# Optimization experiments

Measured on AMD Instinct MI355X. Metric: run time of the kernel, lower is better.

## Reference

```python
import jax, jax.numpy as jnp
import numpy as np
import math

B, N, M = 4, 2048, 2048
DIM_Q = DIM_K = DIM_V = 1024
H = 16

def setup_inputs() -> dict:
    key = jax.random.key(0)
    ks = jax.random.split(key, 10)
    s = 0.02
    return {
        "Q": jax.random.normal(ks[0], (B, N, DIM_Q), jnp.float32),
        "K": jax.random.normal(ks[1], (B, M, DIM_K), jnp.float32),
        "Wq": jax.random.normal(ks[2], (DIM_V, DIM_Q), jnp.float32) * s,
        "bq": jax.random.normal(ks[3], (DIM_V,), jnp.float32) * s,
        "Wk": jax.random.normal(ks[4], (DIM_V, DIM_K), jnp.float32) * s,
        "bk": jax.random.normal(ks[5], (DIM_V,), jnp.float32) * s,
        "Wv": jax.random.normal(ks[6], (DIM_V, DIM_K), jnp.float32) * s,
        "bv": jax.random.normal(ks[7], (DIM_V,), jnp.float32) * s,
        "Wo": jax.random.normal(ks[8], (DIM_V, DIM_V), jnp.float32) * s,
        "bo": jax.random.normal(ks[9], (DIM_V,), jnp.float32) * s,
    }

def reference(Q, K, Wq, bq, Wk, bk, Wv, bv, Wo, bo):
    d = DIM_V // H  # head dim
    Qp = Q @ Wq.T + bq            # [B,N,DIM_V]
    Kp = K @ Wk.T + bk            # [B,M,DIM_V]
    Vp = K @ Wv.T + bv            # [B,M,DIM_V]
    # split heads: [B,T,H,d] -> [B,H,T,d]
    Qh = Qp.reshape(B, N, H, d).transpose(0, 2, 1, 3)
    Kh = Kp.reshape(B, M, H, d).transpose(0, 2, 1, 3)
    Vh = Vp.reshape(B, M, H, d).transpose(0, 2, 1, 3)
    # NOTE: original scales by sqrt(dim_V), not sqrt(head_dim)
    scores = jnp.einsum('bhnd,bhmd->bhnm', Qh, Kh) / math.sqrt(DIM_V)
    A = jax.nn.softmax(scores, axis=-1)
    Oh = Qh + jnp.einsum('bhnm,bhmd->bhnd', A, Vh)   # residual with projected Q
    O = Oh.transpose(0, 2, 1, 3).reshape(B, N, DIM_V)
    O = O + jax.nn.relu(O @ Wo.T + bo)
    return O
```

## Files before the change

kernel.cpp:

```cpp
#include <hip/hip_runtime.h>
#include <cstddef>
#include <cstdint>


typedef unsigned short ushort_t;
typedef __attribute__((ext_vector_type(8))) short bf16x8;
typedef __attribute__((ext_vector_type(4))) float floatx4;
typedef __attribute__((ext_vector_type(2))) float f32x2;
typedef __attribute__((ext_vector_type(2))) __bf16 b16x2;
typedef __attribute__((ext_vector_type(4))) unsigned short us4;

__device__ __forceinline__ ushort_t f2bf(float x) {
  union { float f; unsigned u; } v; v.f = x;
  unsigned r = v.u + 0x7FFFu + ((v.u >> 16) & 1u);
  return (ushort_t)(r >> 16);
}
__device__ __forceinline__ float bf2f(ushort_t x) {
  union { unsigned u; float f; } v; v.u = ((unsigned)x) << 16;
  return v.f;
}
__device__ __forceinline__ unsigned pk2(float a, float b) {
  union { float f; unsigned u; } x, y; x.f = a; y.f = b;
  return __builtin_amdgcn_perm(y.u + 0x8000u, x.u + 0x8000u, 0x07060302u);
}
__device__ __forceinline__ unsigned pk2c(float a, float b) {
  union { b16x2 v; unsigned u; } r;
  r.v = __builtin_convertvector((f32x2){a, b}, b16x2);
  return r.u;
}
__device__ __forceinline__ floatx4 mfma16(bf16x8 a, bf16x8 b, floatx4 c) {
  return __builtin_amdgcn_mfma_f32_16x16x32_bf16(a, b, c, 0, 0, 0);
}
__device__ __forceinline__ void gld_lds16(const void* g, void* l) {
  __builtin_amdgcn_global_load_lds(
      (const __attribute__((address_space(1))) unsigned int*)g,
      (__attribute__((address_space(3))) unsigned int*)l, 16, 0, 0);
}

__global__ void cvt6(const float* __restrict__ i0, const float* __restrict__ i1,
                     const float* __restrict__ i2, const float* __restrict__ i3,
                     const float* __restrict__ i4, const float* __restrict__ i5,
                     ushort_t* __restrict__ o0, ushort_t* __restrict__ o1,
                     ushort_t* __restrict__ o2, ushort_t* __restrict__ o3,
                     ushort_t* __restrict__ o4, ushort_t* __restrict__ o5) {
  int z = blockIdx.z;
  const float* in = z == 0 ? i0 : z == 1 ? i1 : z == 2 ? i2 : z == 3 ? i3 : z == 4 ? i4 : i5;
  ushort_t* out = z == 0 ? o0 : z == 1 ? o1 : z == 2 ? o2 : z == 3 ? o3 : z == 4 ? o4 : o5;
  int n8 = (z < 2) ? 1048576 : 131072;
  int i = blockIdx.x * 256 + threadIdx.x;
  if (i < n8) {
    const float4* p = (const float4*)in + (size_t)i * 2;
    float4 a = p[0], b = p[1];
    uint4 o;
    o.x = pk2(a.x, a.y); o.y = pk2(a.z, a.w);
    o.z = pk2(b.x, b.y); o.w = pk2(b.z, b.w);
    *((uint4*)out + i) = o;
  }
}

__global__ __launch_bounds__(256, 2)
void gemm_qkv(const ushort_t* __restrict__ Qb, const ushort_t* __restrict__ Kb,
              const ushort_t* __restrict__ Wqb, const ushort_t* __restrict__ Wkb,
              const ushort_t* __restrict__ Wvb,
              const float* __restrict__ bq, const float* __restrict__ bk,
              const float* __restrict__ bv,
              ushort_t* __restrict__ Qp, ushort_t* __restrict__ Kp,
              ushort_t* __restrict__ Vt)
{
  const int Kd = 1024, Nn = 1024;
  const int z = blockIdx.z;
  const ushort_t* Ab = (z == 0) ? Qb : Kb;
  const ushort_t* Bw = (z == 0) ? Wqb : (z == 1) ? Wkb : Wvb;
  const float* bias  = (z == 0) ? bq : (z == 1) ? bk : bv;

  __shared__ __align__(16) ushort_t As[2][8192];
  __shared__ __align__(16) ushort_t Bs[2][8192];
  const int tid = threadIdx.x;
  const int lane = tid & 63, wave = tid >> 6;
  const int wm = (wave >> 1) * 64, wn = (wave & 1) * 64;
  const int rq = lane & 15, kg = lane >> 4;

  const int wg = blockIdx.x, xcd = wg & 7, slot = wg >> 3;
  const int by = xcd * 8 + (slot >> 3);
  const int bx = slot & 7;
  const int row0 = by * 128, col0 = bx * 128;

  const int st_sub = lane >> 3;
  const int st_cs  = (lane & 7) ^ st_sub;

  auto stageAB = [&](int k0, int bufi) {
#pragma unroll
    for (int r = 0; r < 4; ++r) {
      int i = wave * 4 + r;
      int row = i * 8 + st_sub;
      gld_lds16(Ab + (size_t)(row0 + row) * Kd + k0 + st_cs * 8, &As[bufi][i * 512]);
      gld_lds16(Bw + (size_t)(col0 + row) * Kd + k0 + st_cs * 8, &Bs[bufi][i * 512]);
    }
  };

  floatx4 acc[4][4];
#pragma unroll
  for (int i = 0; i < 4; ++i)
#pragma unroll
    for (int j = 0; j < 4; ++j) acc[i][j] = (floatx4){0.f, 0.f, 0.f, 0.f};

  stageAB(0, 0);
  __syncthreads();

  int cur = 0;
  for (int kt = 0; kt < 16; ++kt) {
    if (kt < 15) stageAB((kt + 1) * 64, cur ^ 1);
#pragma unroll
    for (int kq = 0; kq < 2; ++kq) {
      bf16x8 af[4], bfr[4];
#pragma unroll
      for (int mi = 0; mi < 4; ++mi)
        af[mi] = *(const bf16x8*)&As[cur][(wm + mi*16 + rq) * 64 + (((kq*4 + kg) ^ (rq & 7)) * 8)];
#pragma unroll
      for (int ni = 0; ni < 4; ++ni)
        bfr[ni] = *(const bf16x8*)&Bs[cur][(wn + ni*16 + rq) * 64 + (((kq*4 + kg) ^ (rq & 7)) * 8)];
#pragma unroll
      for (int mi = 0; mi < 4; ++mi)
#pragma unroll
        for (int ni = 0; ni < 4; ++ni)
          acc[mi][ni] = mfma16(af[mi], bfr[ni], acc[mi][ni]);
    }
    __syncthreads();
    cur ^= 1;
  }

  float bv4[4];
#pragma unroll
  for (int ni = 0; ni < 4; ++ni) bv4[ni] = bias[col0 + wn + ni*16 + rq];

  if (z < 2) {
    ushort_t* Cb = (z == 0) ? Qp : Kp;
#pragma unroll
    for (int mi = 0; mi < 4; ++mi)
#pragma unroll
      for (int ni = 0; ni < 4; ++ni)
#pragma unroll
        for (int rr = 0; rr < 4; ++rr) {
          int row = row0 + wm + mi*16 + kg*4 + rr;
          int col = col0 + wn + ni*16 + rq;
          Cb[(size_t)row * Nn + col] = f2bf(acc[mi][ni][rr] + bv4[ni]);
        }
  } else {
#pragma unroll
    for (int mi = 0; mi < 4; ++mi)
#pragma unroll
      for (int ni = 0; ni < 4; ++ni) {
        int col = col0 + wn + ni*16 + rq;
        int h = col >> 6, dvb = (col >> 4) & 3;
        int kvg = row0 + wm + (mi >> 1) * 32;
        int bI = kvg >> 11, kv = kvg & 2047;
        int t = kv >> 7, c = (kv >> 5) & 3;
        size_t addr = (size_t)(bI * 16 + h) * 131072 + t * 8192
                    + (c * 4 + dvb) * 512 + (kg * 16 + rq) * 8 + (mi & 1) * 4;
        us4 o = { f2bf(acc[mi][ni][0] + bv4[ni]), f2bf(acc[mi][ni][1] + bv4[ni]),
                  f2bf(acc[mi][ni][2] + bv4[ni]), f2bf(acc[mi][ni][3] + bv4[ni]) };
        *(us4*)(Vt + addr) = o;
      }
  }
}

__global__ __launch_bounds__(256, 2)
void gemm_out(const ushort_t* __restrict__ Ob, const ushort_t* __restrict__ Bw,
              const float* __restrict__ bias, float* __restrict__ Out)
{
  const int Kd = 1024, Nn = 1024;
  __shared__ __align__(16) ushort_t As[2][8192];
  __shared__ __align__(16) ushort_t Bs[2][8192];
  const int tid = threadIdx.x;
  const int lane = tid & 63, wave = tid >> 6;
  const int wm = (wave >> 1) * 64, wn = (wave & 1) * 64;
  const int rq = lane & 15, kg = lane >> 4;

  const int wg = blockIdx.x, xcd = wg & 7, slot = wg >> 3;
  const int by = xcd * 8 + (slot >> 3);
  const int bx = slot & 7;
  const int row0 = by * 128, col0 = bx * 128;

  const int st_sub = lane >> 3;
  const int st_cs  = (lane & 7) ^ st_sub;

  auto stageAB = [&](int k0, int bufi) {
#pragma unroll
    for (int r = 0; r < 4; ++r) {
      int i = wave * 4 + r;
      int row = i * 8 + st_sub;
      gld_lds16(Ob + (size_t)(row0 + row) * Kd + k0 + st_cs * 8, &As[bufi][i * 512]);
      gld_lds16(Bw + (size_t)(col0 + row) * Kd + k0 + st_cs * 8, &Bs[bufi][i * 512]);
    }
  };

  floatx4 acc[4][4];
#pragma unroll
  for (int i = 0; i < 4; ++i)
#pragma unroll
    for (int j = 0; j < 4; ++j) acc[i][j] = (floatx4){0.f, 0.f, 0.f, 0.f};

  stageAB(0, 0);
  __syncthreads();

  int cur = 0;
  for (int kt = 0; kt < 16; ++kt) {
    if (kt < 15) stageAB((kt + 1) * 64, cur ^ 1);
#pragma unroll
    for (int kq = 0; kq < 2; ++kq) {
      bf16x8 af[4], bfr[4];
#pragma unroll
      for (int mi = 0; mi < 4; ++mi)
        af[mi] = *(const bf16x8*)&As[cur][(wm + mi*16 + rq) * 64 + (((kq*4 + kg) ^ (rq & 7)) * 8)];
#pragma unroll
      for (int ni = 0; ni < 4; ++ni)
        bfr[ni] = *(const bf16x8*)&Bs[cur][(wn + ni*16 + rq) * 64 + (((kq*4 + kg) ^ (rq & 7)) * 8)];
#pragma unroll
      for (int mi = 0; mi < 4; ++mi)
#pragma unroll
        for (int ni = 0; ni < 4; ++ni)
          acc[mi][ni] = mfma16(af[mi], bfr[ni], acc[mi][ni]);
    }
    __syncthreads();
    cur ^= 1;
  }

  float bv4[4];
#pragma unroll
  for (int ni = 0; ni < 4; ++ni) bv4[ni] = bias[col0 + wn + ni*16 + rq];
#pragma unroll
  for (int mi = 0; mi < 4; ++mi)
#pragma unroll
    for (int ni = 0; ni < 4; ++ni)
#pragma unroll
      for (int rr = 0; rr < 4; ++rr) {
        int row = row0 + wm + mi*16 + kg*4 + rr;
        int col = col0 + wn + ni*16 + rq;
        size_t idx = (size_t)row * Nn + col;
        float pre = acc[mi][ni][rr] + bv4[ni];
        Out[idx] = bf2f(Ob[idx]) + (pre > 0.f ? pre : 0.f);
      }
}

__global__ __launch_bounds__(256, 2)
void attn_kernel(const ushort_t* __restrict__ Qp,
                 const ushort_t* __restrict__ Kp,
                 const ushort_t* __restrict__ Vt,
                 ushort_t* __restrict__ Ob)
{
  const float sc2 = 0.045084439f;
  const int wg = blockIdx.x, xcd = wg & 7, slot = wg >> 3;
  const int bh = xcd * 8 + (slot >> 4);
  const int qt = slot & 15;
  const int b = bh >> 4, h = bh & 15;
  const int q0 = qt * 128;

  __shared__ __align__(16) ushort_t Ks[2][8192];

  const int tid = threadIdx.x, lane = tid & 63, wq = tid >> 6;
  const int rq = lane & 15, kg = lane >> 4;

  const size_t qkbase = (size_t)(b * 2048) * 1024 + h * 64;
  const ushort_t* vbase = Vt + (size_t)bh * 131072 + lane * 8;

  const int sg_sub = lane >> 3;
  const int sg_csk = (lane & 7) ^ sg_sub;

#pragma unroll
  for (int r = 0; r < 4; ++r) {
    int i = wq * 4 + r;
    int row = i * 8 + sg_sub;
    gld_lds16(Qp + qkbase + (size_t)(q0 + row) * 1024 + sg_csk * 8, &Ks[1][i * 512]);
  }
  __syncthreads();

  auto stage = [&](int kt, int bufi) {
    const int kv0 = kt * 128;
#pragma unroll
    for (int r = 0; r < 4; ++r) {
      int i = wq * 4 + r;
      int rowk = i * 8 + sg_sub;
      gld_lds16(Kp + qkbase + (size_t)(kv0 + rowk) * 1024 + sg_csk * 8,
                &Ks[bufi][i * 512]);
    }
  };
  stage(0, 0);

  bf16x8 aq[2][2];
#pragma unroll
  for (int ni = 0; ni < 2; ++ni)
#pragma unroll
    for (int kq = 0; kq < 2; ++kq) {
      int row = wq * 32 + ni * 16 + rq;
      int ch = (kq * 4 + kg) ^ (rq & 7);
      bf16x8 t = *(const bf16x8*)&Ks[1][row * 64 + ch * 8];
#pragma unroll
      for (int e = 0; e < 8; ++e)
        t[e] = (short)f2bf(bf2f((ushort_t)t[e]) * sc2);
      aq[ni][kq] = t;
    }

  bf16x8 ones;
#pragma unroll
  for (int e = 0; e < 8; ++e) ones[e] = (short)0x3F80;

  const floatx4 zf = (floatx4){0.f, 0.f, 0.f, 0.f};

  floatx4 oacc[2][4];
  floatx4 lacc[2];
#pragma unroll
  for (int nb = 0; nb < 2; ++nb) {
    lacc[nb] = (floatx4){0.f,0.f,0.f,0.f};
#pragma unroll
    for (int dvb = 0; dvb < 4; ++dvb) oacc[nb][dvb] = (floatx4){0.f,0.f,0.f,0.f};
  }

  __syncthreads();

  int cur = 0;
#pragma unroll 2
  for (int kt = 0; kt < 16; ++kt) {
    const ushort_t* vtile = vbase + kt * 8192;

    bf16x8 vfa[16];
#pragma unroll
    for (int j = 0; j < 16; ++j)
      vfa[j] = *(const bf16x8*)(vtile + j * 512);

    if (kt < 15) stage(kt + 1, cur ^ 1);

    floatx4 s[8][2];
    __builtin_amdgcn_s_setprio(1);
    {
      bf16x8 ak[8];
#pragma unroll
      for (int mi = 0; mi < 8; ++mi)
        ak[mi] = *(const bf16x8*)&Ks[cur][(mi * 16 + rq) * 64 + ((kg ^ (rq & 7)) * 8)];
#pragma unroll
      for (int mi = 0; mi < 8; ++mi)
#pragma unroll
        for (int ni = 0; ni < 2; ++ni)
          s[mi][ni] = mfma16(ak[mi], aq[ni][0], zf);
#pragma unroll
      for (int mi = 0; mi < 8; ++mi)
        ak[mi] = *(const bf16x8*)&Ks[cur][(mi * 16 + rq) * 64 + (((4 + kg) ^ (rq & 7)) * 8)];
#pragma unroll
      for (int mi = 0; mi < 8; ++mi)
#pragma unroll
        for (int ni = 0; ni < 2; ++ni)
          s[mi][ni] = mfma16(ak[mi], aq[ni][1], s[mi][ni]);
    }
    __builtin_amdgcn_s_setprio(0);

#pragma unroll
    for (int mi = 0; mi < 2; ++mi)
#pragma unroll
      for (int ni = 0; ni < 2; ++ni)
#pragma unroll
        for (int rr = 0; rr < 4; ++rr)
          s[mi][ni][rr] = __builtin_amdgcn_exp2f(s[mi][ni][rr]);

#pragma unroll
    for (int c = 0; c < 4; ++c) {
      union { unsigned u[4]; bf16x8 v; } pa0, pa1;
      pa0.u[0] = pk2c(s[2*c  ][0][0], s[2*c  ][0][1]);
      pa0.u[1] = pk2c(s[2*c  ][0][2], s[2*c  ][0][3]);
      pa0.u[2] = pk2c(s[2*c+1][0][0], s[2*c+1][0][1]);
      pa0.u[3] = pk2c(s[2*c+1][0][2], s[2*c+1][0][3]);
      pa1.u[0] = pk2c(s[2*c  ][1][0], s[2*c  ][1][1]);
      pa1.u[1] = pk2c(s[2*c  ][1][2], s[2*c  ][1][3]);
      pa1.u[2] = pk2c(s[2*c+1][1][0], s[2*c+1][1][1]);
      pa1.u[3] = pk2c(s[2*c+1][1][2], s[2*c+1][1][3]);
      __builtin_amdgcn_s_setprio(1);
#pragma unroll
      for (int dvb = 0; dvb < 4; ++dvb) {
        oacc[0][dvb] = mfma16(pa0.v, vfa[c*4+dvb], oacc[0][dvb]);
        oacc[1][dvb] = mfma16(pa1.v, vfa[c*4+dvb], oacc[1][dvb]);
      }
      lacc[0] = mfma16(pa0.v, ones, lacc[0]);
      lacc[1] = mfma16(pa1.v, ones, lacc[1]);
      __builtin_amdgcn_s_setprio(0);
      if (c < 3) {
#pragma unroll
        for (int mi = 2*c + 2; mi < 2*c + 4; ++mi)
#pragma unroll
          for (int ni = 0; ni < 2; ++ni)
#pragma unroll
            for (int rr = 0; rr < 4; ++rr)
              s[mi][ni][rr] = __builtin_amdgcn_exp2f(s[mi][ni][rr]);
      }
    }

    __syncthreads();
    cur ^= 1;
  }

#pragma unroll
  for (int nb = 0; nb < 2; ++nb)
#pragma unroll
    for (int rr = 0; rr < 4; ++rr) {
      int row = wq * 32 + nb * 16 + kg * 4 + rr;
      float linv = 1.0f / lacc[nb][rr];
#pragma unroll
      for (int dvb = 0; dvb < 4; ++dvb) {
        int col = dvb * 16 + rq;
        size_t idx = qkbase + (size_t)(q0 + row) * 1024 + col;
        Ob[idx] = f2bf(oacc[nb][dvb][rr] * linv + bf2f(Qp[idx]));
      }
    }
}

extern "C" void kernel_launch(void* const* d_in, const int* in_sizes, int n_in,
                              void* d_out, int out_size, void* d_ws, size_t ws_size,
                              hipStream_t stream)
{
  const float* Q  = (const float*)d_in[0];
  const float* K  = (const float*)d_in[1];
  const float* Wq = (const float*)d_in[2];
  const float* bq = (const float*)d_in[3];
  const float* Wk = (const float*)d_in[4];
  const float* bk = (const float*)d_in[5];
  const float* Wv = (const float*)d_in[6];
  const float* bv = (const float*)d_in[7];
  const float* Wo = (const float*)d_in[8];
  const float* bo = (const float*)d_in[9];
  float* Out = (float*)d_out;

  ushort_t* ws = (ushort_t*)d_ws;
  const size_t E = (size_t)8192 * 1024;
  const size_t WSZ = (size_t)1024 * 1024;
  ushort_t* Qb  = ws;
  ushort_t* Kb  = ws + E;
  ushort_t* Qp  = ws + 2*E;
  ushort_t* Kp  = ws + 3*E;
  ushort_t* Vt  = ws + 4*E;
  ushort_t* Wqb = ws + 5*E;
  ushort_t* Wkb = ws + 5*E + WSZ;
  ushort_t* Wvb = ws + 5*E + 2*WSZ;
  ushort_t* Wob = ws + 5*E + 3*WSZ;
  ushort_t* Ob  = Qb;

  cvt6<<<dim3(4096, 1, 6), 256, 0, stream>>>(Q, K, Wq, Wk, Wv, Wo,
                                             Qb, Kb, Wqb, Wkb, Wvb, Wob);

  dim3 blk(256);
  gemm_qkv<<<dim3(512, 1, 3), blk, 0, stream>>>(Qb, Kb, Wqb, Wkb, Wvb,
                                                bq, bk, bv, Qp, Kp, Vt);
  attn_kernel<<<dim3(1024), blk, 0, stream>>>(Qp, Kp, Vt, Ob);
  gemm_out<<<dim3(512), blk, 0, stream>>>(Ob, Wob, bo, Out);
}
```

Before: 277.5 us.

## Split attention key tile into two halves to cut registers and raise occupancy

Each 128-key tile in the attention inner loop is now processed as two 64-key halves. Scores, exp and the PV MFMAs run per half, and the V fragments are loaded in two batches of 8 instead of 16 at once. The manual unroll of 2 is dropped and launch bounds rise from 2 to 3 waves-per-SIMD occupancy, so the compiler must fit more waves per CU. This risks spills or exposed V global-load latency, because the second V batch is fetched mid-iteration with less time to hide it.

```diff
diff --git a/kernel.cpp b/kernel.cpp
--- a/kernel.cpp
+++ b/kernel.cpp
@@ -242,7 +242,7 @@
       }
 }
 
-__global__ __launch_bounds__(256, 2)
+__global__ __launch_bounds__(256, 3)
 void attn_kernel(const ushort_t* __restrict__ Qp,
                  const ushort_t* __restrict__ Kp,
                  const ushort_t* __restrict__ Vt,
@@ -318,50 +318,54 @@
   __syncthreads();
 
   int cur = 0;
-#pragma unroll 2
   for (int kt = 0; kt < 16; ++kt) {
     const ushort_t* vtile = vbase + kt * 8192;
-
-    bf16x8 vfa[16];
-#pragma unroll
-    for (int j = 0; j < 16; ++j)
-      vfa[j] = *(const bf16x8*)(vtile + j * 512);
+    const ushort_t* kc = &Ks[cur][0];
+
+    bf16x8 vf0[8];
+#pragma unroll
+    for (int j = 0; j < 8; ++j)
+      vf0[j] = *(const bf16x8*)(vtile + j * 512);
 
     if (kt < 15) stage(kt + 1, cur ^ 1);
 
-    floatx4 s[8][2];
+    floatx4 s[4][2];
     __builtin_amdgcn_s_setprio(1);
     {
-      bf16x8 ak[8];
-#pragma unroll
-      for (int mi = 0; mi < 8; ++mi)
-        ak[mi] = *(const bf16x8*)&Ks[cur][(mi * 16 + rq) * 64 + ((kg ^ (rq & 7)) * 8)];
-#pragma unroll
-      for (int mi = 0; mi < 8; ++mi)
+      bf16x8 ak[4];
+#pragma unroll
+      for (int mi = 0; mi < 4; ++mi)
+        ak[mi] = *(const bf16x8*)&kc[(mi * 16 + rq) * 64 + ((kg ^ (rq & 7)) * 8)];
+#pragma unroll
+      for (int mi = 0; mi < 4; ++mi)
 #pragma unroll
         for (int ni = 0; ni < 2; ++ni)
           s[mi][ni] = mfma16(ak[mi], aq[ni][0], zf);
 #pragma unroll
-      for (int mi = 0; mi < 8; ++mi)
-        ak[mi] = *(const bf16x8*)&Ks[cur][(mi * 16 + rq) * 64 + (((4 + kg) ^ (rq & 7)) * 8)];
-#pragma unroll
-      for (int mi = 0; mi < 8; ++mi)
+      for (int mi = 0; mi < 4; ++mi)
+        ak[mi] = *(const bf16x8*)&kc[(mi * 16 + rq) * 64 + (((4 + kg) ^ (rq & 7)) * 8)];
+#pragma unroll
+      for (int mi = 0; mi < 4; ++mi)
 #pragma unroll
         for (int ni = 0; ni < 2; ++ni)
           s[mi][ni] = mfma16(ak[mi], aq[ni][1], s[mi][ni]);
     }
     __builtin_amdgcn_s_setprio(0);
 
-#pragma unroll
-    for (int mi = 0; mi < 2; ++mi)
+    bf16x8 vf1[8];
+#pragma unroll
+    for (int j = 0; j < 8; ++j)
+      vf1[j] = *(const bf16x8*)(vtile + (8 + j) * 512);
+
+#pragma unroll
+    for (int mi = 0; mi < 4; ++mi)
 #pragma unroll
       for (int ni = 0; ni < 2; ++ni)
 #pragma unroll
         for (int rr = 0; rr < 4; ++rr)
           s[mi][ni][rr] = __builtin_amdgcn_exp2f(s[mi][ni][rr]);
-
-#pragma unroll
-    for (int c = 0; c < 4; ++c) {
+#pragma unroll
+    for (int c = 0; c < 2; ++c) {
       union { unsigned u[4]; bf16x8 v; } pa0, pa1;
       pa0.u[0] = pk2c(s[2*c  ][0][0], s[2*c  ][0][1]);
       pa0.u[1] = pk2c(s[2*c  ][0][2], s[2*c  ][0][3]);
@@ -374,21 +378,63 @@
       __builtin_amdgcn_s_setprio(1);
 #pragma unroll
       for (int dvb = 0; dvb < 4; ++dvb) {
-        oacc[0][dvb] = mfma16(pa0.v, vfa[c*4+dvb], oacc[0][dvb]);
-        oacc[1][dvb] = mfma16(pa1.v, vfa[c*4+dvb], oacc[1][dvb]);
+        oacc[0][dvb] = mfma16(pa0.v, vf0[c*4+dvb], oacc[0][dvb]);
+        oacc[1][dvb] = mfma16(pa1.v, vf0[c*4+dvb], oacc[1][dvb]);
       }
       lacc[0] = mfma16(pa0.v, ones, lacc[0]);
       lacc[1] = mfma16(pa1.v, ones, lacc[1]);
       __builtin_amdgcn_s_setprio(0);
-      if (c < 3) {
-#pragma unroll
-        for (int mi = 2*c + 2; mi < 2*c + 4; ++mi)
-#pragma unroll
-          for (int ni = 0; ni < 2; ++ni)
-#pragma unroll
-            for (int rr = 0; rr < 4; ++rr)
-              s[mi][ni][rr] = __builtin_amdgcn_exp2f(s[mi][ni][rr]);
+    }
+
+    __builtin_amdgcn_s_setprio(1);
+    {
+      bf16x8 ak[4];
+#pragma unroll
+      for (int mi = 0; mi < 4; ++mi)
+        ak[mi] = *(const bf16x8*)&kc[((4 + mi) * 16 + rq) * 64 + ((kg ^ (rq & 7)) * 8)];
+#pragma unroll
+      for (int mi = 0; mi < 4; ++mi)
+#pragma unroll
+        for (int ni = 0; ni < 2; ++ni)
+          s[mi][ni] = mfma16(ak[mi], aq[ni][0], zf);
+#pragma unroll
+      for (int mi = 0; mi < 4; ++mi)
+        ak[mi] = *(const bf16x8*)&kc[((4 + mi) * 16 + rq) * 64 + (((4 + kg) ^ (rq & 7)) * 8)];
+#pragma unroll
+      for (int mi = 0; mi < 4; ++mi)
+#pragma unroll
+        for (int ni = 0; ni < 2; ++ni)
+          s[mi][ni] = mfma16(ak[mi], aq[ni][1], s[mi][ni]);
+    }
+    __builtin_amdgcn_s_setprio(0);
+
+#pragma unroll
+    for (int mi = 0; mi < 4; ++mi)
+#pragma unroll
+      for (int ni = 0; ni < 2; ++ni)
+#pragma unroll
+        for (int rr = 0; rr < 4; ++rr)
+          s[mi][ni][rr] = __builtin_amdgcn_exp2f(s[mi][ni][rr]);
+#pragma unroll
+    for (int c = 0; c < 2; ++c) {
+      union { unsigned u[4]; bf16x8 v; } pa0, pa1;
+      pa0.u[0] = pk2c(s[2*c  ][0][0], s[2*c  ][0][1]);
+      pa0.u[1] = pk2c(s[2*c  ][0][2], s[2*c  ][0][3]);
+      pa0.u[2] = pk2c(s[2*c+1][0][0], s[2*c+1][0][1]);
+      pa0.u[3] = pk2c(s[2*c+1][0][2], s[2*c+1][0][3]);
+      pa1.u[0] = pk2c(s[2*c  ][1][0], s[2*c  ][1][1]);
+      pa1.u[1] = pk2c(s[2*c  ][1][2], s[2*c  ][1][3]);
+      pa1.u[2] = pk2c(s[2*c+1][1][0], s[2*c+1][1][1]);
+      pa1.u[3] = pk2c(s[2*c+1][1][2], s[2*c+1][1][3]);
+      __builtin_amdgcn_s_setprio(1);
+#pragma unroll
+      for (int dvb = 0; dvb < 4; ++dvb) {
+        oacc[0][dvb] = mfma16(pa0.v, vf1[c*4+dvb], oacc[0][dvb]);
+        oacc[1][dvb] = mfma16(pa1.v, vf1[c*4+dvb], oacc[1][dvb]);
       }
+      lacc[0] = mfma16(pa0.v, ones, lacc[0]);
+      lacc[1] = mfma16(pa1.v, ones, lacc[1]);
+      __builtin_amdgcn_s_setprio(0);
     }
 
     __syncthreads();
```

Result: slower. 335.6 us (+20.9%).

## Load K fragments directly from global memory instead of staging through LDS

Applied to the files above, without the earlier changes.

The attention kernel stops staging Q and K tiles through double-buffered shared memory with async global-to-LDS copies and barriers. Each wave now reads its K and Q MFMA fragments straight from global memory and splits each 128-key tile into two 64-key halves to cut register pressure. This removes LDS traffic and __syncthreads, but the four waves now each re-read the same K rows through cache with strided 16-byte accesses and no prefetch overlap. The exp2 interleaving with the PV MFMAs is also simplified. It also leaves an unused kfr pointer.

```diff
diff --git a/kernel.cpp b/kernel.cpp
--- a/kernel.cpp
+++ b/kernel.cpp
@@ -255,45 +255,20 @@
   const int b = bh >> 4, h = bh & 15;
   const int q0 = qt * 128;
 
-  __shared__ __align__(16) ushort_t Ks[2][8192];
-
   const int tid = threadIdx.x, lane = tid & 63, wq = tid >> 6;
   const int rq = lane & 15, kg = lane >> 4;
 
   const size_t qkbase = (size_t)(b * 2048) * 1024 + h * 64;
   const ushort_t* vbase = Vt + (size_t)bh * 131072 + lane * 8;
-
-  const int sg_sub = lane >> 3;
-  const int sg_csk = (lane & 7) ^ sg_sub;
-
-#pragma unroll
-  for (int r = 0; r < 4; ++r) {
-    int i = wq * 4 + r;
-    int row = i * 8 + sg_sub;
-    gld_lds16(Qp + qkbase + (size_t)(q0 + row) * 1024 + sg_csk * 8, &Ks[1][i * 512]);
-  }
-  __syncthreads();
-
-  auto stage = [&](int kt, int bufi) {
-    const int kv0 = kt * 128;
-#pragma unroll
-    for (int r = 0; r < 4; ++r) {
-      int i = wq * 4 + r;
-      int rowk = i * 8 + sg_sub;
-      gld_lds16(Kp + qkbase + (size_t)(kv0 + rowk) * 1024 + sg_csk * 8,
-                &Ks[bufi][i * 512]);
-    }
-  };
-  stage(0, 0);
+  const ushort_t* kfr = Kp + qkbase + (size_t)kg * 32;
 
   bf16x8 aq[2][2];
 #pragma unroll
   for (int ni = 0; ni < 2; ++ni)
 #pragma unroll
     for (int kq = 0; kq < 2; ++kq) {
-      int row = wq * 32 + ni * 16 + rq;
-      int ch = (kq * 4 + kg) ^ (rq & 7);
-      bf16x8 t = *(const bf16x8*)&Ks[1][row * 64 + ch * 8];
+      int row = q0 + wq * 32 + ni * 16 + rq;
+      bf16x8 t = *(const bf16x8*)(Qp + qkbase + (size_t)row * 1024 + (kq * 4 + kg) * 8);
 #pragma unroll
       for (int e = 0; e < 8; ++e)
         t[e] = (short)f2bf(bf2f((ushort_t)t[e]) * sc2);
@@ -315,84 +290,69 @@
     for (int dvb = 0; dvb < 4; ++dvb) oacc[nb][dvb] = (floatx4){0.f,0.f,0.f,0.f};
   }
 
-  __syncthreads();
-
-  int cur = 0;
-#pragma unroll 2
   for (int kt = 0; kt < 16; ++kt) {
+    const int kv0 = kt * 128;
     const ushort_t* vtile = vbase + kt * 8192;
 
-    bf16x8 vfa[16];
-#pragma unroll
-    for (int j = 0; j < 16; ++j)
-      vfa[j] = *(const bf16x8*)(vtile + j * 512);
-
-    if (kt < 15) stage(kt + 1, cur ^ 1);
-
-    floatx4 s[8][2];
-    __builtin_amdgcn_s_setprio(1);
-    {
-      bf16x8 ak[8];
-#pragma unroll
-      for (int mi = 0; mi < 8; ++mi)
-        ak[mi] = *(const bf16x8*)&Ks[cur][(mi * 16 + rq) * 64 + ((kg ^ (rq & 7)) * 8)];
-#pragma unroll
-      for (int mi = 0; mi < 8; ++mi)
+#pragma unroll
+    for (int hf = 0; hf < 2; ++hf) {
+      bf16x8 ak[2][4];
+#pragma unroll
+      for (int kq = 0; kq < 2; ++kq)
+#pragma unroll
+        for (int mi = 0; mi < 4; ++mi) {
+          int kv = kv0 + hf * 64 + mi * 16 + rq;
+          ak[kq][mi] = *(const bf16x8*)(Kp + qkbase + (size_t)kv * 1024 + (kq * 4 + kg) * 8);
+        }
+      bf16x8 vf[8];
+#pragma unroll
+      for (int j = 0; j < 8; ++j)
+        vf[j] = *(const bf16x8*)(vtile + (hf * 8 + j) * 512);
+
+      floatx4 s[4][2];
+      __builtin_amdgcn_s_setprio(1);
+#pragma unroll
+      for (int mi = 0; mi < 4; ++mi)
 #pragma unroll
         for (int ni = 0; ni < 2; ++ni)
-          s[mi][ni] = mfma16(ak[mi], aq[ni][0], zf);
-#pragma unroll
-      for (int mi = 0; mi < 8; ++mi)
-        ak[mi] = *(const bf16x8*)&Ks[cur][(mi * 16 + rq) * 64 + (((4 + kg) ^ (rq & 7)) * 8)];
-#pragma unroll
-      for (int mi = 0; mi < 8; ++mi)
+          s[mi][ni] = mfma16(ak[0][mi], aq[ni][0], zf);
+#pragma unroll
+      for (int mi = 0; mi < 4; ++mi)
 #pragma unroll
         for (int ni = 0; ni < 2; ++ni)
-          s[mi][ni] = mfma16(ak[mi], aq[ni][1], s[mi][ni]);
-    }
-    __builtin_amdgcn_s_setprio(0);
-
-#pragma unroll
-    for (int mi = 0; mi < 2; ++mi)
-#pragma unroll
-      for (int ni = 0; ni < 2; ++ni)
-#pragma unroll
-        for (int rr = 0; rr < 4; ++rr)
-          s[mi][ni][rr] = __builtin_amdgcn_exp2f(s[mi][ni][rr]);
-
-#pragma unroll
-    for (int c = 0; c < 4; ++c) {
-      union { unsigned u[4]; bf16x8 v; } pa0, pa1;
-      pa0.u[0] = pk2c(s[2*c  ][0][0], s[2*c  ][0][1]);
-      pa0.u[1] = pk2c(s[2*c  ][0][2], s[2*c  ][0][3]);
-      pa0.u[2] = pk2c(s[2*c+1][0][0], s[2*c+1][0][1]);
-      pa0.u[3] = pk2c(s[2*c+1][0][2], s[2*c+1][0][3]);
-      pa1.u[0] = pk2c(s[2*c  ][1][0], s[2*c  ][1][1]);
-      pa1.u[1] = pk2c(s[2*c  ][1][2], s[2*c  ][1][3]);
-      pa1.u[2] = pk2c(s[2*c+1][1][0], s[2*c+1][1][1]);
-      pa1.u[3] = pk2c(s[2*c+1][1][2], s[2*c+1][1][3]);
-      __builtin_amdgcn_s_setprio(1);
-#pragma unroll
-      for (int dvb = 0; dvb < 4; ++dvb) {
-        oacc[0][dvb] = mfma16(pa0.v, vfa[c*4+dvb], oacc[0][dvb]);
-        oacc[1][dvb] = mfma16(pa1.v, vfa[c*4+dvb], oacc[1][dvb]);
+          s[mi][ni] = mfma16(ak[1][mi], aq[ni][1], s[mi][ni]);
+      __builtin_amdgcn_s_setprio(0);
+
+#pragma unroll
+      for (int mi = 0; mi < 4; ++mi)
+#pragma unroll
+        for (int ni = 0; ni < 2; ++ni)
+#pragma unroll
+          for (int rr = 0; rr < 4; ++rr)
+            s[mi][ni][rr] = __builtin_amdgcn_exp2f(s[mi][ni][rr]);
+
+#pragma unroll
+      for (int c = 0; c < 2; ++c) {
+        union { unsigned u[4]; bf16x8 v; } pa0, pa1;
+        pa0.u[0] = pk2c(s[2*c  ][0][0], s[2*c  ][0][1]);
+        pa0.u[1] = pk2c(s[2*c  ][0][2], s[2*c  ][0][3]);
+        pa0.u[2] = pk2c(s[2*c+1][0][0], s[2*c+1][0][1]);
+        pa0.u[3] = pk2c(s[2*c+1][0][2], s[2*c+1][0][3]);
+        pa1.u[0] = pk2c(s[2*c  ][1][0], s[2*c  ][1][1]);
+        pa1.u[1] = pk2c(s[2*c  ][1][2], s[2*c  ][1][3]);
+        pa1.u[2] = pk2c(s[2*c+1][1][0], s[2*c+1][1][1]);
+        pa1.u[3] = pk2c(s[2*c+1][1][2], s[2*c+1][1][3]);
+        __builtin_amdgcn_s_setprio(1);
+#pragma unroll
+        for (int dvb = 0; dvb < 4; ++dvb) {
+          oacc[0][dvb] = mfma16(pa0.v, vf[c*4+dvb], oacc[0][dvb]);
+          oacc[1][dvb] = mfma16(pa1.v, vf[c*4+dvb], oacc[1][dvb]);
+        }
+        lacc[0] = mfma16(pa0.v, ones, lacc[0]);
+        lacc[1] = mfma16(pa1.v, ones, lacc[1]);
+        __builtin_amdgcn_s_setprio(0);
       }
-      lacc[0] = mfma16(pa0.v, ones, lacc[0]);
-      lacc[1] = mfma16(pa1.v, ones, lacc[1]);
-      __builtin_amdgcn_s_setprio(0);
-      if (c < 3) {
-#pragma unroll
-        for (int mi = 2*c + 2; mi < 2*c + 4; ++mi)
-#pragma unroll
-          for (int ni = 0; ni < 2; ++ni)
-#pragma unroll
-            for (int rr = 0; rr < 4; ++rr)
-              s[mi][ni][rr] = __builtin_amdgcn_exp2f(s[mi][ni][rr]);
-      }
-    }
-
-    __syncthreads();
-    cur ^= 1;
+    }
   }
 
 #pragma unroll
```

Result: slower. 360.7 us (+30.0%).
